# Kernel optimization log

Hardware: AMD Instinct MI355X
Metric: run time of the kernel (lower is better)

The kernel has to match this reference:

```python
import jax, jax.numpy as jnp
import numpy as np

BLOCK = 64  # bitsandbytes 4-bit blocksize
OUT, IN = 4096, 4096
# NF4 codebook (bitsandbytes values)
NF4_CODE = np.array([
    -1.0, -0.6961928009986877, -0.5250730514526367, -0.39491748809814453,
    -0.28444138169288635, -0.18477343022823334, -0.09105003625154495, 0.0,
    0.07958029955625534, 0.16093020141124725, 0.24611230194568634,
    0.33791524171829224, 0.44070982933044434, 0.5626170039176941,
    0.7229568362236023, 1.0], dtype=np.float32)


def setup_inputs() -> dict:
    key = jax.random.key(0)
    k1, k2, k3 = jax.random.split(key, 3)
    x = jax.random.normal(k1, (8, 2048, IN), dtype=jnp.float32)
    qweight = jax.random.randint(k2, (OUT * IN,), 0, 16, dtype=jnp.int32)
    absmax = jax.random.uniform(k3, (OUT * IN // BLOCK,), dtype=jnp.float32)
    return {"x": x, "qweight": qweight, "absmax": absmax}


def reference(x, qweight, absmax):
    code = jnp.asarray(NF4_CODE)
    # dequantize: codebook lookup, then per-block absmax scaling
    w = code[qweight].reshape(-1, BLOCK) * absmax[:, None]  # [n_blocks, BLOCK]
    W = w.reshape(OUT, IN)                                   # [out, in]
    # linear: y = x @ W^T  (no bias: quantized_bias is None)
    return jnp.einsum('bsi,oi->bso', x, W)
```

## Files before the change

### kernel.cpp

```cpp
#include <hip/hip_runtime.h>
#include <hip/hip_bf16.h>
#include <stdint.h>

#define IN_DIM  4096
#define OUT_DIM 4096
#define M_DIM   16384
#define BK      64
#define NT      (IN_DIM / BK)

typedef float f32x4 __attribute__((ext_vector_type(4)));
typedef short bf16x8 __attribute__((ext_vector_type(8)));
typedef short bf16x4 __attribute__((ext_vector_type(4)));
typedef int   i32x4 __attribute__((ext_vector_type(4)));

__device__ __constant__ float NF4_CODE_D[16] = {
    -1.0f, -0.6961928009986877f, -0.5250730514526367f, -0.39491748809814453f,
    -0.28444138169288635f, -0.18477343022823334f, -0.09105003625154495f, 0.0f,
    0.07958029955625534f, 0.16093020141124725f, 0.24611230194568634f,
    0.33791524171829224f, 0.44070982933044434f, 0.5626170039176941f,
    0.7229568362236023f, 1.0f};

static __device__ __forceinline__ ushort f2bf(float f) {
  union { float f; uint32_t u; } v; v.f = f;
  uint32_t r = v.u + 0x7FFFu + ((v.u >> 16) & 1u);
  return (ushort)(r >> 16);
}

__global__ void dequant_nf4(const int* __restrict__ q, const float* __restrict__ am,
                            ushort* __restrict__ w) {
  __shared__ float code[16];
  if (threadIdx.x < 16) code[threadIdx.x] = NF4_CODE_D[threadIdx.x];
  __syncthreads();
  size_t t = (size_t)blockIdx.x * blockDim.x + threadIdx.x;
  size_t base = t * 8;
  i32x4 qa = *(const i32x4*)(q + base);
  i32x4 qb = *(const i32x4*)(q + base + 4);
  float s = am[base >> 6];
  bf16x8 o;
  o[0] = (short)f2bf(code[qa[0] & 15] * s);
  o[1] = (short)f2bf(code[qa[1] & 15] * s);
  o[2] = (short)f2bf(code[qa[2] & 15] * s);
  o[3] = (short)f2bf(code[qa[3] & 15] * s);
  o[4] = (short)f2bf(code[qb[0] & 15] * s);
  o[5] = (short)f2bf(code[qb[1] & 15] * s);
  o[6] = (short)f2bf(code[qb[2] & 15] * s);
  o[7] = (short)f2bf(code[qb[3] & 15] * s);
  *(bf16x8*)(w + base) = o;
}

__global__ void cvt_x(const float* __restrict__ x, ushort* __restrict__ xb) {
  size_t t = (size_t)blockIdx.x * blockDim.x + threadIdx.x;
  size_t base = t * 8;
  f32x4 a = *(const f32x4*)(x + base);
  f32x4 b = *(const f32x4*)(x + base + 4);
  bf16x8 o;
  o[0] = (short)f2bf(a[0]); o[1] = (short)f2bf(a[1]);
  o[2] = (short)f2bf(a[2]); o[3] = (short)f2bf(a[3]);
  o[4] = (short)f2bf(b[0]); o[5] = (short)f2bf(b[1]);
  o[6] = (short)f2bf(b[2]); o[7] = (short)f2bf(b[3]);
  *(bf16x8*)(xb + base) = o;
}

static __device__ __forceinline__ void llds16(const ushort* g, ushort* l) {
  __builtin_amdgcn_global_load_lds(
      (const __attribute__((address_space(1))) void*)g,
      (__attribute__((address_space(3))) void*)l, 16, 0, 0);
}

__global__ __launch_bounds__(512, 2) void gemm256(const ushort* __restrict__ Xb,
                                                  const ushort* __restrict__ W,
                                                  float* __restrict__ Y) {
  __shared__ ushort As[2][256 * BK];
  __shared__ ushort Bs[2][256 * BK];

  const int tid  = threadIdx.x;
  const int lane = tid & 63;
  const int wid  = tid >> 6;
  const int wr   = wid >> 2;
  const int wc   = wid & 3;
  const int l15  = lane & 15;
  const int kg   = lane >> 4;
  const int l7   = lane & 7;

  const int bid = blockIdx.x;
  const int wg  = (bid & 7) * 128 + (bid >> 3);
  const int tm  = wg >> 4;
  const int tn  = wg & 15;
  const size_t row0 = (size_t)tm * 256;
  const size_t col0 = (size_t)tn * 256;

  const int srow  = tid >> 3;
  const int scol8 = ((tid & 7) ^ (srow & 7)) * 8;
  const int wbase = wid << 9;

  f32x4  acc[8][4] = {};
  bf16x8 a[4][2], b0[2][2], b1[2][2];

#define BARX()  asm volatile("s_barrier" ::: "memory")
#define VMC4()  asm volatile("s_waitcnt vmcnt(4)" ::: "memory")
#define VMC0()  asm volatile("s_waitcnt vmcnt(0)" ::: "memory")
#define PRI1()  __builtin_amdgcn_s_setprio(1)
#define PRI0()  __builtin_amdgcn_s_setprio(0)

#define STAGE_A(kt, h, nb) do { \
    llds16(Xb + (row0 + (h)*128 +  0 + srow) * IN_DIM + (kt)*BK + scol8, \
           &As[nb][(h)*8192 +    0 + wbase]); \
    llds16(Xb + (row0 + (h)*128 + 64 + srow) * IN_DIM + (kt)*BK + scol8, \
           &As[nb][(h)*8192 + 4096 + wbase]); \
  } while (0)

#define STAGE_B(kt, h, nb) do { \
    llds16(W + (col0 + (h)*128 +  0 + srow) * IN_DIM + (kt)*BK + scol8, \
           &Bs[nb][(h)*8192 +    0 + wbase]); \
    llds16(W + (col0 + (h)*128 + 64 + srow) * IN_DIM + (kt)*BK + scol8, \
           &Bs[nb][(h)*8192 + 4096 + wbase]); \
  } while (0)

#define LDA(nb, mh) do { \
    _Pragma("unroll") for (int mi = 0; mi < 4; ++mi) \
    _Pragma("unroll") for (int ks = 0; ks < 2; ++ks) \
      a[mi][ks] = *(const bf16x8*)&As[nb][(wr*128 + (mh)*64 + mi*16 + l15) * BK \
                                          + (((ks*4 + kg) ^ l7) * 8)]; \
  } while (0)

#define LDB(nb, nh, bb) do { \
    _Pragma("unroll") for (int ni = 0; ni < 2; ++ni) \
    _Pragma("unroll") for (int ks = 0; ks < 2; ++ks) \
      bb[ni][ks] = *(const bf16x8*)&Bs[nb][(wc*64 + (nh)*32 + ni*16 + l15) * BK \
                                           + (((ks*4 + kg) ^ l7) * 8)]; \
  } while (0)

#define QUAD(mh, nh, bb) do { \
    _Pragma("unroll") for (int mi = 0; mi < 4; ++mi) \
    _Pragma("unroll") for (int ni = 0; ni < 2; ++ni) \
    _Pragma("unroll") for (int ks = 0; ks < 2; ++ks) \
      acc[(mh)*4 + mi][(nh)*2 + ni] = __builtin_amdgcn_mfma_f32_16x16x32_bf16( \
          a[mi][ks], bb[ni][ks], acc[(mh)*4 + mi][(nh)*2 + ni], 0, 0, 0); \
  } while (0)

#define KTILE(cur, tA, tB) do { \
    LDA(cur, 0); LDB(cur, 0, b0); STAGE_A(tA, 0, (cur)^1); \
    BARX(); PRI1(); QUAD(0, 0, b0); PRI0(); BARX(); \
    LDB(cur, 1, b1); STAGE_A(tA, 1, (cur)^1); \
    BARX(); PRI1(); QUAD(0, 1, b1); PRI0(); BARX(); \
    LDA(cur, 1); STAGE_B(tB, 0, cur); \
    BARX(); PRI1(); QUAD(1, 1, b1); PRI0(); BARX(); \
    STAGE_B(tB, 1, cur); \
    BARX(); PRI1(); QUAD(1, 0, b0); PRI0(); VMC4(); BARX(); \
  } while (0)

  STAGE_B(0, 0, 0); STAGE_B(0, 1, 0);
  STAGE_A(0, 0, 0); STAGE_A(0, 1, 0);
  STAGE_B(1, 0, 1); STAGE_B(1, 1, 1);
  VMC4(); BARX();

#pragma unroll 1
  for (int t = 0; t < NT - 3; t += 2) {
    KTILE(0, t + 1, t + 2);
    KTILE(1, t + 2, t + 3);
  }

  LDA(0, 0); LDB(0, 0, b0); STAGE_A(NT - 1, 0, 1);
  BARX(); PRI1(); QUAD(0, 0, b0); PRI0(); BARX();
  LDB(0, 1, b1); STAGE_A(NT - 1, 1, 1);
  BARX(); PRI1(); QUAD(0, 1, b1); PRI0(); BARX();
  LDA(0, 1);
  BARX(); PRI1(); QUAD(1, 1, b1); PRI0(); BARX();
  BARX(); PRI1(); QUAD(1, 0, b0); PRI0(); VMC0(); BARX();

  LDA(1, 0); LDB(1, 0, b0); LDB(1, 1, b1);
  QUAD(0, 0, b0); QUAD(0, 1, b1);
  LDA(1, 1);
  QUAD(1, 1, b1); QUAD(1, 0, b0);

#undef KTILE
#undef QUAD
#undef LDB
#undef LDA
#undef STAGE_B
#undef STAGE_A

  float* yb = Y + (row0 + wr * 128 + kg * 4) * OUT_DIM + col0 + wc * 64 + l15;
#pragma unroll
  for (int m = 0; m < 8; ++m)
#pragma unroll
    for (int n = 0; n < 4; ++n)
#pragma unroll
      for (int v = 0; v < 4; ++v)
        yb[(size_t)(m * 16 + v) * OUT_DIM + n * 16] = acc[m][n][v];
}

__global__ void gemm_fb(const float* __restrict__ X, const ushort* __restrict__ W,
                        float* __restrict__ Y) {
  __shared__ ushort Af[128 * 64];
  __shared__ ushort Bf[128 * 64];
  const int tid  = threadIdx.x;
  const int lane = tid & 63;
  const int wid  = tid >> 6;
  const int wr   = wid >> 1, wc = wid & 1;
  const int bid  = blockIdx.x;
  const int tm   = bid / 32, tn = bid % 32;
  const size_t row0 = (size_t)tm * 128, col0 = (size_t)tn * 128;
  f32x4 acc[4][4] = {};
  const int arow = lane & 15, kgrp = lane >> 4;
  const int srow = lane >> 3, scol = (lane & 7) * 8;
  for (int k0 = 0; k0 < IN_DIM; k0 += 64) {
    f32x4 r[8];
#pragma unroll
    for (int i = 0; i < 8; ++i)
      r[i] = *(const f32x4*)(X + (row0 + i * 16 + (tid >> 4)) * IN_DIM + k0 + (tid & 15) * 4);
#pragma unroll
    for (int i = 0; i < 8; ++i) {
      bf16x4 o;
      o[0] = (short)f2bf(r[i][0]); o[1] = (short)f2bf(r[i][1]);
      o[2] = (short)f2bf(r[i][2]); o[3] = (short)f2bf(r[i][3]);
      *(bf16x4*)&Af[(i * 16 + (tid >> 4)) * 64 + (tid & 15) * 4] = o;
    }
#pragma unroll
    for (int i = 0; i < 4; ++i) {
      const int c = wid * 4 + i;
      llds16(W + (col0 + c * 8 + srow) * IN_DIM + k0 + scol, Bf + c * 512);
    }
    __syncthreads();
#pragma unroll
    for (int ks = 0; ks < 2; ++ks) {
      bf16x8 a[4], b[4];
#pragma unroll
      for (int m = 0; m < 4; ++m)
        a[m] = *(const bf16x8*)&Af[(wr * 64 + m * 16 + arow) * 64 + ks * 32 + kgrp * 8];
#pragma unroll
      for (int n = 0; n < 4; ++n)
        b[n] = *(const bf16x8*)&Bf[(wc * 64 + n * 16 + arow) * 64 + ks * 32 + kgrp * 8];
#pragma unroll
      for (int m = 0; m < 4; ++m)
#pragma unroll
        for (int n = 0; n < 4; ++n)
          acc[m][n] = __builtin_amdgcn_mfma_f32_16x16x32_bf16(a[m], b[n], acc[m][n], 0, 0, 0);
    }
    __syncthreads();
  }
  float* yb = Y + (row0 + wr * 64) * OUT_DIM + col0 + wc * 64;
  const int crow = (lane >> 4) * 4, ccol = lane & 15;
#pragma unroll
  for (int m = 0; m < 4; ++m)
#pragma unroll
    for (int n = 0; n < 4; ++n)
#pragma unroll
      for (int v = 0; v < 4; ++v)
        yb[(size_t)(m * 16 + crow + v) * OUT_DIM + n * 16 + ccol] = acc[m][n][v];
}

extern "C" void kernel_launch(void* const* d_in, const int* in_sizes, int n_in,
                              void* d_out, int out_size, void* d_ws, size_t ws_size,
                              hipStream_t stream) {
  const float* x  = (const float*)d_in[0];
  const int*   q  = (const int*)d_in[1];
  const float* am = (const float*)d_in[2];
  float* y = (float*)d_out;

  ushort* w = (ushort*)d_ws;
  const size_t WB = (size_t)OUT_DIM * IN_DIM * sizeof(ushort);
  const size_t XB = (size_t)M_DIM * IN_DIM * sizeof(ushort);

  dequant_nf4<<<(OUT_DIM * (size_t)IN_DIM) / 8 / 256, 256, 0, stream>>>(q, am, w);

  if (ws_size >= WB + XB) {
    ushort* xb = (ushort*)((char*)d_ws + WB);
    cvt_x<<<((size_t)M_DIM * IN_DIM) / 8 / 256, 256, 0, stream>>>(x, xb);
    gemm256<<<(M_DIM / 256) * (OUT_DIM / 256), 512, 0, stream>>>(xb, w, y);
  } else {
    gemm_fb<<<(M_DIM / 128) * (OUT_DIM / 128), 256, 0, stream>>>(x, w, y);
  }
}
```

Measured before the change: 633.6 us.

## Restructure GEMM main loop with split-half warp mapping and register double-buffered A fragments

Rewrites the main K loop to run one k-tile per iteration with A/B LDS fragments prefetched into separate register sets (aA/aB). The next tile's first fragments are loaded at the end of each iteration, and staging of the next A/B halves is interleaved between the MFMA quads with adjusted vmcnt waits. The warp-to-tile mapping also changes so that each half-tile (mh/nh) spans 128 rows/cols and warps interleave inside it, which changes the LDS read pattern and the output store layout. The aim is to hide LDS read latency and global-load latency behind MFMAs. In exchange it uses more VGPRs for the extra fragment buffer and relies on the new waitcnt counts being correct.

```diff
diff --git a/kernel.cpp b/kernel.cpp
--- a/kernel.cpp
+++ b/kernel.cpp
@@ -94,11 +94,10 @@
   const int wbase = wid << 9;
 
   f32x4  acc[8][4] = {};
-  bf16x8 a[4][2], b0[2][2], b1[2][2];
-
-#define BARX()  asm volatile("s_barrier" ::: "memory")
-#define VMC4()  asm volatile("s_waitcnt vmcnt(4)" ::: "memory")
-#define VMC0()  asm volatile("s_waitcnt vmcnt(0)" ::: "memory")
+  bf16x8 aA[4][2], aB[4][2], b0[2][2], b1[2][2];
+
+#define BARX()  __builtin_amdgcn_s_barrier()
+#define VMC(n)  asm volatile("s_waitcnt vmcnt(" #n ")" ::: "memory")
 #define PRI1()  __builtin_amdgcn_s_setprio(1)
 #define PRI0()  __builtin_amdgcn_s_setprio(0)
 
@@ -116,78 +115,84 @@
            &Bs[nb][(h)*8192 + 4096 + wbase]); \
   } while (0)
 
-#define LDA(nb, mh) do { \
+#define LDA_(dst, nb, mh) do { \
     _Pragma("unroll") for (int mi = 0; mi < 4; ++mi) \
     _Pragma("unroll") for (int ks = 0; ks < 2; ++ks) \
-      a[mi][ks] = *(const bf16x8*)&As[nb][(wr*128 + (mh)*64 + mi*16 + l15) * BK \
-                                          + (((ks*4 + kg) ^ l7) * 8)]; \
-  } while (0)
-
-#define LDB(nb, nh, bb) do { \
+      dst[mi][ks] = *(const bf16x8*)&As[nb][((mh)*128 + wr*64 + mi*16 + l15) * BK \
+                                            + (((ks*4 + kg) ^ l7) * 8)]; \
+  } while (0)
+
+#define LDB_(dst, nb, nh) do { \
     _Pragma("unroll") for (int ni = 0; ni < 2; ++ni) \
     _Pragma("unroll") for (int ks = 0; ks < 2; ++ks) \
-      bb[ni][ks] = *(const bf16x8*)&Bs[nb][(wc*64 + (nh)*32 + ni*16 + l15) * BK \
-                                           + (((ks*4 + kg) ^ l7) * 8)]; \
-  } while (0)
-
-#define QUAD(mh, nh, bb) do { \
+      dst[ni][ks] = *(const bf16x8*)&Bs[nb][((nh)*128 + wc*32 + ni*16 + l15) * BK \
+                                            + (((ks*4 + kg) ^ l7) * 8)]; \
+  } while (0)
+
+#define QUAD(mh, nh, aR, bR) do { PRI1(); \
     _Pragma("unroll") for (int mi = 0; mi < 4; ++mi) \
     _Pragma("unroll") for (int ni = 0; ni < 2; ++ni) \
     _Pragma("unroll") for (int ks = 0; ks < 2; ++ks) \
       acc[(mh)*4 + mi][(nh)*2 + ni] = __builtin_amdgcn_mfma_f32_16x16x32_bf16( \
-          a[mi][ks], bb[ni][ks], acc[(mh)*4 + mi][(nh)*2 + ni], 0, 0, 0); \
-  } while (0)
-
-#define KTILE(cur, tA, tB) do { \
-    LDA(cur, 0); LDB(cur, 0, b0); STAGE_A(tA, 0, (cur)^1); \
-    BARX(); PRI1(); QUAD(0, 0, b0); PRI0(); BARX(); \
-    LDB(cur, 1, b1); STAGE_A(tA, 1, (cur)^1); \
-    BARX(); PRI1(); QUAD(0, 1, b1); PRI0(); BARX(); \
-    LDA(cur, 1); STAGE_B(tB, 0, cur); \
-    BARX(); PRI1(); QUAD(1, 1, b1); PRI0(); BARX(); \
-    STAGE_B(tB, 1, cur); \
-    BARX(); PRI1(); QUAD(1, 0, b0); PRI0(); VMC4(); BARX(); \
-  } while (0)
-
+          aR[mi][ks], bR[ni][ks], acc[(mh)*4 + mi][(nh)*2 + ni], 0, 0, 0); \
+    PRI0(); } while (0)
+
+  STAGE_A(0, 0, 0); STAGE_A(0, 1, 0);
   STAGE_B(0, 0, 0); STAGE_B(0, 1, 0);
-  STAGE_A(0, 0, 0); STAGE_A(0, 1, 0);
-  STAGE_B(1, 0, 1); STAGE_B(1, 1, 1);
-  VMC4(); BARX();
+  STAGE_A(1, 0, 1);
+  VMC(2); BARX();
+  LDA_(aA, 0, 0); LDB_(b0, 0, 0);
 
 #pragma unroll 1
-  for (int t = 0; t < NT - 3; t += 2) {
-    KTILE(0, t + 1, t + 2);
-    KTILE(1, t + 2, t + 3);
+  for (int t = 0; t < NT - 1; ++t) {
+    const int cur = t & 1, nxt = cur ^ 1;
+    STAGE_A(t + 1, 1, nxt);
+    VMC(4); BARX();
+    LDB_(b1, cur, 1); LDA_(aB, cur, 1);
+    QUAD(0, 0, aA, b0);
+    STAGE_B(t + 1, 0, nxt);
+    BARX();
+    QUAD(0, 1, aA, b1);
+    STAGE_B(t + 1, 1, nxt);
+    BARX();
+    QUAD(1, 1, aB, b1);
+    if (t < NT - 2) {
+      STAGE_A(t + 2, 0, cur);
+      VMC(4);
+    } else {
+      VMC(2);
+    }
+    BARX();
+    QUAD(1, 0, aB, b0);
+    LDA_(aA, nxt, 0); LDB_(b0, nxt, 0);
   }
 
-  LDA(0, 0); LDB(0, 0, b0); STAGE_A(NT - 1, 0, 1);
-  BARX(); PRI1(); QUAD(0, 0, b0); PRI0(); BARX();
-  LDB(0, 1, b1); STAGE_A(NT - 1, 1, 1);
-  BARX(); PRI1(); QUAD(0, 1, b1); PRI0(); BARX();
-  LDA(0, 1);
-  BARX(); PRI1(); QUAD(1, 1, b1); PRI0(); BARX();
-  BARX(); PRI1(); QUAD(1, 0, b0); PRI0(); VMC0(); BARX();
-
-  LDA(1, 0); LDB(1, 0, b0); LDB(1, 1, b1);
-  QUAD(0, 0, b0); QUAD(0, 1, b1);
-  LDA(1, 1);
-  QUAD(1, 1, b1); QUAD(1, 0, b0);
-
-#undef KTILE
+  VMC(0); BARX();
+  LDB_(b1, 1, 1); LDA_(aB, 1, 1);
+  QUAD(0, 0, aA, b0);
+  QUAD(0, 1, aA, b1);
+  QUAD(1, 1, aB, b1);
+  QUAD(1, 0, aB, b0);
+
 #undef QUAD
-#undef LDB
-#undef LDA
+#undef LDB_
+#undef LDA_
 #undef STAGE_B
 #undef STAGE_A
 
-  float* yb = Y + (row0 + wr * 128 + kg * 4) * OUT_DIM + col0 + wc * 64 + l15;
-#pragma unroll
-  for (int m = 0; m < 8; ++m)
-#pragma unroll
-    for (int n = 0; n < 4; ++n)
-#pragma unroll
-      for (int v = 0; v < 4; ++v)
-        yb[(size_t)(m * 16 + v) * OUT_DIM + n * 16] = acc[m][n][v];
+  float* yb = Y + (row0 + wr * 64 + kg * 4) * OUT_DIM + col0 + wc * 32 + l15;
+#pragma unroll
+  for (int mh = 0; mh < 2; ++mh)
+#pragma unroll
+    for (int mi = 0; mi < 4; ++mi)
+#pragma unroll
+      for (int nh = 0; nh < 2; ++nh)
+#pragma unroll
+        for (int ni = 0; ni < 2; ++ni)
+#pragma unroll
+          for (int v = 0; v < 4; ++v)
+            yb[(size_t)(mh * 128 + mi * 16 + v) * OUT_DIM + nh * 128 + ni * 16] =
+                acc[mh * 4 + mi][nh * 2 + ni][v];
 }
 
 __global__ void gemm_fb(const float* __restrict__ X, const ushort* __restrict__ W,
```

After: 584.7 us. -7.7%, faster.
